# Performance work log

Hardware: AMD Instinct MI355X
Metric: run time of the kernel (lower is better)

The kernel has to match this reference:

```python
import jax, jax.numpy as jnp
import numpy as np

C = 256
CQK = C // 8  # query/key channels from Conv2d(in_dim, in_dim//8, 1)


def _cross_attn(x, y, qw, qb, kw, kb, vw, vb, gamma):
    # x, y: [B, C, H, W]; 1x1 convs are channel matmuls
    B, Cc, H, W = x.shape
    N = H * W
    xf = x.reshape(B, Cc, N)
    yf = y.reshape(B, Cc, N)
    q = jnp.einsum('oc,bcn->bno', qw, xf) + qb  # [B, N, CQK]
    k = jnp.einsum('oc,bcn->bon', kw, yf) + kb[:, None]  # [B, CQK, N]
    energy = jnp.einsum('bnc,bcm->bnm', q, k)  # [B, N, N]
    attn = jax.nn.softmax(energy, axis=2)
    v = jnp.einsum('oc,bcn->bon', vw, yf) + vb[:, None]  # [B, C, N]
    out = jnp.einsum('bcm,bnm->bcn', v, attn)  # value @ attention^T
    out = out.reshape(B, Cc, H, W)
    return gamma * out + x


def setup_inputs() -> dict:
    key = jax.random.key(0)
    ks = jax.random.split(key, 16)
    B, H, W = 4, 64, 64
    s = 1.0 / np.sqrt(C)
    d = {
        'x': jax.random.normal(ks[0], (B, C, H, W), jnp.float32),
        'y': jax.random.normal(ks[1], (B, C, H, W), jnp.float32),
        'z': jax.random.normal(ks[2], (B, C, H, W), jnp.float32),
        'q1_w': jax.random.normal(ks[3], (CQK, C), jnp.float32) * s,
        'q1_b': jax.random.normal(ks[4], (CQK,), jnp.float32) * s,
        'k1_w': jax.random.normal(ks[5], (CQK, C), jnp.float32) * s,
        'k1_b': jax.random.normal(ks[6], (CQK,), jnp.float32) * s,
        'v1_w': jax.random.normal(ks[7], (C, C), jnp.float32) * s,
        'v1_b': jax.random.normal(ks[8], (C,), jnp.float32) * s,
        'gamma1': jax.random.normal(ks[9], (1,), jnp.float32) * 0.1,
        'q2_w': jax.random.normal(ks[10], (CQK, C), jnp.float32) * s,
        'q2_b': jax.random.normal(ks[11], (CQK,), jnp.float32) * s,
        'k2_w': jax.random.normal(ks[12], (CQK, C), jnp.float32) * s,
        'k2_b': jax.random.normal(ks[13], (CQK,), jnp.float32) * s,
        'v2_w': jax.random.normal(ks[14], (C, C), jnp.float32) * s,
        'v2_b': jax.random.normal(ks[15], (C,), jnp.float32) * s,
        'gamma2': jax.random.normal(jax.random.fold_in(key, 99), (1,), jnp.float32) * 0.1,
    }
    return d


def reference(x, y, z, q1_w, q1_b, k1_w, k1_b, v1_w, v1_b, gamma1,
              q2_w, q2_b, k2_w, k2_b, v2_w, v2_b, gamma2):
    out1 = _cross_attn(x, y, q1_w, q1_b, k1_w, k1_b, v1_w, v1_b, gamma1)
    out2 = _cross_attn(out1, z, q2_w, q2_b, k2_w, k2_b, v2_w, v2_b, gamma2)
    return out2
```

## Files before the change

kernel.cpp:

```cpp
#include <hip/hip_runtime.h>
#include <hip/hip_bf16.h>

#define NSEQ 4096
#define CDIM 256
#define CQKD 32
#define LOG2E 1.4426950408889634f

typedef float v4f __attribute__((ext_vector_type(4)));
typedef float v16f __attribute__((ext_vector_type(16)));
typedef short v8s __attribute__((ext_vector_type(8)));
typedef unsigned long long u64;

__device__ __forceinline__ float exp2_(float x) {
#if __has_builtin(__builtin_amdgcn_exp2f)
  return __builtin_amdgcn_exp2f(x);
#else
  float r;
  __asm__("v_exp_f32 %0, %1" : "=v"(r) : "v"(x));
  return r;
#endif
}

__device__ __forceinline__ unsigned short f2bf(float x) {
  unsigned u = __builtin_bit_cast(unsigned, x);
  unsigned r = (u + 0x7FFFu + ((u >> 16) & 1u)) >> 16;
  return (unsigned short)r;
}
__device__ __forceinline__ float bf2f(unsigned short s) {
  unsigned u = ((unsigned)s) << 16;
  return __builtin_bit_cast(float, u);
}
__device__ __forceinline__ unsigned int pack_bf16(float a, float b) {
#if __has_builtin(__builtin_amdgcn_cvt_pk_bf16_f32)
  typedef __bf16 v2bf __attribute__((ext_vector_type(2)));
  v2bf r = __builtin_amdgcn_cvt_pk_bf16_f32(a, b);
  return __builtin_bit_cast(unsigned int, r);
#else
  return ((unsigned)f2bf(b) << 16) | (unsigned)f2bf(a);
#endif
}

__device__ __forceinline__ unsigned char f2e4m3(float x) {
  unsigned u = __builtin_bit_cast(unsigned, x);
  unsigned s = (u >> 24) & 0x80u;
  unsigned au = u & 0x7fffffffu;
  if (au > 0x43e00000u) return (unsigned char)(s | 0x7eu);
  if (au < 0x3c800000u) {
    float ax = __builtin_bit_cast(float, au);
    int q = (int)(ax * 512.0f + 0.5f);
    if (q > 7) q = 7;
    return (unsigned char)(s | (unsigned)q);
  }
  int e = (int)((au >> 23) & 0xffu) - 127 + 7;
  unsigned m = au & 0x7fffffu;
  unsigned mr = m + 0x7ffffu + ((m >> 20) & 1u);
  if (mr >= 0x800000u) { mr -= 0x800000u; e += 1; if (e >= 16) return (unsigned char)(s | 0x7e); }
  return (unsigned char)(s | ((unsigned)e << 3) | (mr >> 20));
}
__device__ __forceinline__ unsigned int pack4_fp8(float a, float b, float c, float d) {
#if __has_builtin(__builtin_amdgcn_cvt_pk_fp8_f32)
  int v = 0;
  v = __builtin_amdgcn_cvt_pk_fp8_f32(a, b, v, false);
  v = __builtin_amdgcn_cvt_pk_fp8_f32(c, d, v, true);
  return (unsigned int)v;
#else
  return (unsigned)f2e4m3(a) | ((unsigned)f2e4m3(b) << 8) |
         ((unsigned)f2e4m3(c) << 16) | ((unsigned)f2e4m3(d) << 24);
#endif
}

__device__ __forceinline__ void barrier_lds() {
  __asm__ __volatile__("s_waitcnt lgkmcnt(0)\n\ts_barrier" ::: "memory");
}

__global__ __launch_bounds__(256) void convw_kernel(
    const float* __restrict__ q1w, const float* __restrict__ k1w,
    const float* __restrict__ k2w, const float* __restrict__ q2w,
    const float* __restrict__ v1w, const float* __restrict__ v2w,
    unsigned short* __restrict__ W) {
  const int s = blockIdx.x * 256 + threadIdx.x;
  const float* src;
  int o, ch0;
  size_t obase;
  float scale = 1.0f;
  if (s < 3072) {
    const int wsel = s >> 10, r = s & 1023;
    src = wsel == 0 ? q1w : (wsel == 1 ? k1w : k2w);
    const int ot = r >> 9, cb = (r >> 6) & 7, lane = r & 63;
    o = ot * 16 + (lane & 15);
    ch0 = cb * 32 + ((lane >> 4) & 3) * 8;
    obase = (size_t)wsel * 8192 + (size_t)r * 8;
  } else if (s < 19456) {
    const int s2 = s - 3072, which = s2 >> 13, r = s2 & 8191;
    src = which == 0 ? v1w : v2w;
    const int ot = r >> 9, cb = (r >> 6) & 7, lane = r & 63;
    o = ot * 16 + (lane & 15);
    ch0 = cb * 32 + ((lane >> 4) & 3) * 8;
    obase = 32768 + (size_t)which * 65536 + (size_t)r * 8;
  } else {
    const int r = s - 19456;
    src = q2w;
    const int lane = r & 63;
    o = lane & 31;
    ch0 = (r >> 6) * 16 + (lane >> 5) * 8;
    obase = 24576 + (size_t)r * 8;
    scale = LOG2E;
  }
#pragma unroll
  for (int j = 0; j < 8; ++j)
    W[obase + j] = f2bf(src[o * CDIM + ch0 + j] * scale);
}

__global__ __launch_bounds__(256) void prep_kernel(
    const float* __restrict__ x, const float* __restrict__ y,
    const float* __restrict__ z, const unsigned short* __restrict__ Wbf,
    const float* __restrict__ q1b, const float* __restrict__ k1b,
    const float* __restrict__ k2b, const float* __restrict__ v1b,
    const float* __restrict__ v2b, unsigned short* __restrict__ Q1,
    unsigned short* __restrict__ K1, unsigned short* __restrict__ K2,
    unsigned char* __restrict__ V1, unsigned char* __restrict__ V2) {
  __shared__ unsigned short t[256][72];
  __shared__ unsigned short Kt[64][40];
  const int src = blockIdx.z;
  const float* in = src == 0 ? x : (src == 1 ? y : z);
  const int b = blockIdx.y;
  const int n0 = blockIdx.x * 64;
  const int tid = threadIdx.x, lane = tid & 63, w = tid >> 6;
  const int quad = lane >> 4, r15 = lane & 15, l31 = lane & 31, lh = lane >> 5;
  const float* ip = in + (size_t)(b * CDIM) * NSEQ + n0;
  {
    const int chb = tid >> 4, c4 = (tid & 15) * 4;
#pragma unroll
    for (int p = 0; p < 16; ++p) {
      const int ch = p * 16 + chb;
      float4 v = *(const float4*)(ip + (size_t)ch * NSEQ + c4);
      uint2 pk;
      pk.x = pack_bf16(v.x, v.y);
      pk.y = pack_bf16(v.z, v.w);
      *(uint2*)&t[ch][c4] = pk;
    }
  }
  __syncthreads();
  v8s af[8];
#pragma unroll
  for (int cb = 0; cb < 8; ++cb) {
    union { unsigned short e[8]; v8s v; } u;
#pragma unroll
    for (int j = 0; j < 8; ++j) u.e[j] = t[cb * 32 + quad * 8 + j][w * 16 + r15];
    af[cb] = u.v;
  }
  const int nt = blockIdx.x * 4 + w;
  const unsigned short* Wqk = Wbf + src * 8192;
  v4f a0 = {0.f, 0.f, 0.f, 0.f}, a1 = a0;
#pragma unroll
  for (int cb = 0; cb < 8; ++cb) {
    v8s b0 = *(const v8s*)(Wqk + (size_t)cb * 512 + lane * 8);
    v8s b1 = *(const v8s*)(Wqk + (size_t)(8 + cb) * 512 + lane * 8);
    a0 = __builtin_amdgcn_mfma_f32_16x16x32_bf16(af[cb], b0, a0, 0, 0, 0);
    a1 = __builtin_amdgcn_mfma_f32_16x16x32_bf16(af[cb], b1, a1, 0, 0, 0);
  }
  if (src == 0) {
#pragma unroll
    for (int r = 0; r < 4; ++r) {
      Q1[((size_t)b * NSEQ + nt * 16 + quad * 4 + r) * CQKD + r15] =
          f2bf((a0[r] + q1b[r15]) * LOG2E);
      Q1[((size_t)b * NSEQ + nt * 16 + quad * 4 + r) * CQKD + 16 + r15] =
          f2bf((a1[r] + q1b[16 + r15]) * LOG2E);
    }
    return;
  }
  const float* kbias = src == 1 ? k1b : k2b;
#pragma unroll
  for (int r = 0; r < 4; ++r) {
    Kt[w * 16 + quad * 4 + r][r15] = f2bf(a0[r] + kbias[r15]);
    Kt[w * 16 + quad * 4 + r][16 + r15] = f2bf(a1[r] + kbias[16 + r15]);
  }
  const unsigned short* Wv = Wbf + 32768 + (src - 1) * 65536;
  const float* vbias = src == 1 ? v1b : v2b;
  v4f vacc[16];
#pragma unroll
  for (int ot = 0; ot < 16; ++ot) vacc[ot] = (v4f){0.f, 0.f, 0.f, 0.f};
#pragma unroll
  for (int cb = 0; cb < 8; ++cb) {
    const v8s afc = af[cb];
#pragma unroll
    for (int ot = 0; ot < 16; ++ot) {
      v8s bf = *(const v8s*)(Wv + (size_t)(ot * 8 + cb) * 512 + lane * 8);
      vacc[ot] = __builtin_amdgcn_mfma_f32_16x16x32_bf16(afc, bf, vacc[ot], 0, 0, 0);
    }
  }
  __syncthreads();
  unsigned char* Vt8 = (unsigned char*)t;
#pragma unroll
  for (int ot = 0; ot < 16; ++ot) {
    const int ch = ot * 16 + r15;
    const float bv = vbias[ch];
    *(unsigned int*)&Vt8[(size_t)ch * 72 + w * 16 + quad * 4] =
        pack4_fp8(vacc[ot][0] + bv, vacc[ot][1] + bv, vacc[ot][2] + bv, vacc[ot][3] + bv);
  }
  {
    unsigned short* Kout = (src == 1 ? K1 : K2) + (size_t)b * (NSEQ / 16) * 512;
    *(v8s*)(Kout + ((size_t)nt * 64 + lane) * 8) = *(const v8s*)&Kt[w * 16 + r15][quad * 8];
  }
  __syncthreads();
  unsigned char* Vout = (src == 1 ? V1 : V2) + (size_t)b * (NSEQ / 16) * 8 * 512;
#pragma unroll
  for (int chb = 0; chb < 8; ++chb)
    *(u64*)(Vout + (((size_t)nt * 8 + chb) * 64 + lane) * 8) =
        *(const u64*)&Vt8[(size_t)(chb * 32 + l31) * 72 + w * 16 + lh * 8];
}


__device__ __forceinline__ void max_pass(
    const unsigned short* __restrict__ Kp, const v8s qf[2], int w, int lane,
    float (*lbuf)[32], float m[2]) {
  const v4f vzero4 = {0.f, 0.f, 0.f, 0.f};
  const int r15 = lane & 15;
  const unsigned short* Kl = Kp + (size_t)w * 512 + lane * 8;
  v8s kA = *(const v8s*)(Kl);
  m[0] = -3.0e38f;
  m[1] = -3.0e38f;
  for (int kt = 0; kt < 32; ++kt) {
    v8s kB = *(const v8s*)(Kl + (size_t)((kt + 1) & 31) * 4096);
#pragma unroll
    for (int qt = 0; qt < 2; ++qt) {
      v4f st = __builtin_amdgcn_mfma_f32_16x16x32_bf16(kA, qf[qt], vzero4, 0, 0, 0);
      m[qt] = fmaxf(m[qt], fmaxf(fmaxf(st[0], st[1]), fmaxf(st[2], st[3])));
    }
    kA = kB;
  }
#pragma unroll
  for (int qt = 0; qt < 2; ++qt) {
    m[qt] = fmaxf(m[qt], __shfl_xor(m[qt], 16));
    m[qt] = fmaxf(m[qt], __shfl_xor(m[qt], 32));
  }
  if (lane < 16) {
#pragma unroll
    for (int qt = 0; qt < 2; ++qt) lbuf[w][qt * 16 + lane] = m[qt];
  }
  __syncthreads();
#pragma unroll
  for (int qt = 0; qt < 2; ++qt) {
    float mm = lbuf[0][qt * 16 + r15];
#pragma unroll
    for (int ww = 1; ww < 8; ++ww) mm = fmaxf(mm, lbuf[ww][qt * 16 + r15]);
    m[qt] = mm;
  }
  __syncthreads();
}

__device__ __forceinline__ void attn_tile(
    const unsigned short* __restrict__ Kl, const unsigned char* __restrict__ Vl,
    unsigned char* __restrict__ P, const v8s qf[2], const float m[2], int w, int lane,
    int pbuf, int tn, const v8s kfu, const u64* vfu, v8s& kfn, u64* vfn,
    v16f& acc, float lsum[2]) {
  const v4f vzero4 = {0.f, 0.f, 0.f, 0.f};
  const int quad = (lane >> 4) & 3, r15 = lane & 15;
  const int l31 = lane & 31, lh = lane >> 5;
  kfn = *(const v8s*)(Kl + (size_t)tn * 4096);
#pragma unroll
  for (int s = 0; s < 8; ++s)
    vfn[s] = *(const u64*)(Vl + (size_t)tn * 32768 + s * 4096);
  unsigned char* pw = P + pbuf * 4352 + w * 16 + quad * 4;
#pragma unroll
  for (int qt = 0; qt < 2; ++qt) {
    v4f st = __builtin_amdgcn_mfma_f32_16x16x32_bf16(kfu, qf[qt], vzero4, 0, 0, 0);
    float e0 = exp2_(st[0] - m[qt]), e1 = exp2_(st[1] - m[qt]);
    float e2 = exp2_(st[2] - m[qt]), e3 = exp2_(st[3] - m[qt]);
    lsum[qt] += (e0 + e1) + (e2 + e3);
    *(unsigned int*)(pw + (size_t)(qt * 16 + r15) * 136) = pack4_fp8(e0, e1, e2, e3);
  }
  barrier_lds();
  const unsigned char* pb = P + pbuf * 4352;
#pragma unroll
  for (int s = 0; s < 8; ++s) {
    long pf0 = (long)*(const u64*)(pb + (size_t)l31 * 136 + s * 16 + lh * 8);
    acc = __builtin_amdgcn_mfma_f32_32x32x16_fp8_fp8((long)vfu[s], pf0, acc, 0, 0, 0);
  }
}

__device__ __forceinline__ void attn_loop(
    const unsigned short* __restrict__ Kp, const unsigned char* __restrict__ Vp,
    unsigned char* __restrict__ P, const v8s qf[2], const float m[2], int w, int lane,
    v16f& acc, float lsum[2]) {
  const unsigned short* Kl = Kp + (size_t)w * 512 + lane * 8;
  const unsigned char* Vl = Vp + (size_t)w * 512 + lane * 8;
  v8s kA, kB;
  u64 vA[8], vB[8];
  kA = *(const v8s*)(Kl);
#pragma unroll
  for (int s = 0; s < 8; ++s) vA[s] = *(const u64*)(Vl + (size_t)s * 4096);
  for (int kt = 0; kt < 32; kt += 2) {
    attn_tile(Kl, Vl, P, qf, m, w, lane, 0, (kt + 1) & 31, kA, vA, kB, vB, acc, lsum);
    attn_tile(Kl, Vl, P, qf, m, w, lane, 1, (kt + 2) & 31, kB, vB, kA, vA, acc, lsum);
  }
}

__global__ __launch_bounds__(512, 2) void fused_attn_kernel(
    const unsigned short* __restrict__ Q1g, const unsigned short* __restrict__ K1g,
    const unsigned char* __restrict__ V1g, const unsigned short* __restrict__ K2g,
    const unsigned char* __restrict__ V2g, const unsigned short* __restrict__ W2g,
    const float* __restrict__ x, const float* __restrict__ q2b,
    const float* __restrict__ g1p, const float* __restrict__ g2p,
    float* __restrict__ outp) {
  __shared__ __align__(16) unsigned char P[2 * 4352];
  __shared__ __align__(16) unsigned short out1T[32 * 264];
  __shared__ __align__(16) unsigned short q2s[32 * 32];
  __shared__ float lbuf[8][32];

  const int tid = threadIdx.x;
  const int lane = tid & 63;
  const int w = tid >> 6;
  const int quad = lane >> 4;
  const int r15 = lane & 15;
  const int l31 = lane & 31, lh = lane >> 5;
  const int b = blockIdx.x & 3;
  const int n0 = (blockIdx.x >> 2) * 32;

  const float g1 = g1p[0];
  const float g2 = g2p[0];

  const unsigned short* Qp  = Q1g + (size_t)b * NSEQ * CQKD;
  const unsigned short* K1p = K1g + (size_t)b * (NSEQ / 16) * 512;
  const unsigned short* K2p = K2g + (size_t)b * (NSEQ / 16) * 512;
  const unsigned char* V1p  = V1g + (size_t)b * (NSEQ / 16) * 8 * 512;
  const unsigned char* V2p  = V2g + (size_t)b * (NSEQ / 16) * 8 * 512;

  v8s qf[2];
#pragma unroll
  for (int qt = 0; qt < 2; ++qt)
    qf[qt] = *(const v8s*)(Qp + (n0 + qt * 16 + r15) * CQKD + quad * 8);

  v16f acc = (v16f)(0.f);
  float lsum[2] = {0.f, 0.f};
  float m[2];

  max_pass(K1p, qf, w, lane, lbuf, m);
  attn_loop(K1p, V1p, P, qf, m, w, lane, acc, lsum);
#pragma unroll
  for (int qt = 0; qt < 2; ++qt) {
    lsum[qt] += __shfl_xor(lsum[qt], 16);
    lsum[qt] += __shfl_xor(lsum[qt], 32);
  }
  __syncthreads();
  if (lane < 16) {
#pragma unroll
    for (int qt = 0; qt < 2; ++qt) lbuf[w][qt * 16 + lane] = lsum[qt];
  }
  __syncthreads();
  float rinv;
  {
    float d = 0.f;
#pragma unroll
    for (int ww = 0; ww < 8; ++ww) d += lbuf[ww][l31];
    rinv = 1.0f / d;
  }
  {
    const int q = l31;
#pragma unroll
    for (int rg = 0; rg < 4; ++rg) {
      const int c = w * 32 + 8 * rg + 4 * lh;
      float o0 = g1 * (acc[rg * 4 + 0] * rinv) + x[((size_t)b * CDIM + c + 0) * NSEQ + n0 + q];
      float o1 = g1 * (acc[rg * 4 + 1] * rinv) + x[((size_t)b * CDIM + c + 1) * NSEQ + n0 + q];
      float o2 = g1 * (acc[rg * 4 + 2] * rinv) + x[((size_t)b * CDIM + c + 2) * NSEQ + n0 + q];
      float o3 = g1 * (acc[rg * 4 + 3] * rinv) + x[((size_t)b * CDIM + c + 3) * NSEQ + n0 + q];
      uint2 pk;
      pk.x = pack_bf16(o0, o1);
      pk.y = pack_bf16(o2, o3);
      *(uint2*)(out1T + (size_t)q * 264 + c) = pk;
    }
  }
  __syncthreads();

  if (w == 0) {
    v16f qacc = (v16f)(0.f);
#pragma unroll
    for (int s = 0; s < 16; ++s) {
      v8s af = *(const v8s*)(W2g + (size_t)(s * 64 + lane) * 8);
      v8s bf = *(const v8s*)(out1T + (size_t)l31 * 264 + s * 16 + lh * 8);
      qacc = __builtin_amdgcn_mfma_f32_32x32x16_bf16(af, bf, qacc, 0, 0, 0);
    }
#pragma unroll
    for (int rg = 0; rg < 4; ++rg) {
      const int o = 8 * rg + 4 * lh;
      uint2 pk;
      pk.x = pack_bf16(qacc[rg * 4 + 0] + q2b[o + 0] * LOG2E, qacc[rg * 4 + 1] + q2b[o + 1] * LOG2E);
      pk.y = pack_bf16(qacc[rg * 4 + 2] + q2b[o + 2] * LOG2E, qacc[rg * 4 + 3] + q2b[o + 3] * LOG2E);
      *(uint2*)(q2s + (size_t)l31 * 32 + o) = pk;
    }
  }
  __syncthreads();

#pragma unroll
  for (int qt = 0; qt < 2; ++qt)
    qf[qt] = *(const v8s*)(q2s + (qt * 16 + r15) * 32 + quad * 8);
  acc = (v16f)(0.f);
  lsum[0] = 0.f;
  lsum[1] = 0.f;
  max_pass(K2p, qf, w, lane, lbuf, m);
  attn_loop(K2p, V2p, P, qf, m, w, lane, acc, lsum);
#pragma unroll
  for (int qt = 0; qt < 2; ++qt) {
    lsum[qt] += __shfl_xor(lsum[qt], 16);
    lsum[qt] += __shfl_xor(lsum[qt], 32);
  }
  __syncthreads();
  if (lane < 16) {
#pragma unroll
    for (int qt = 0; qt < 2; ++qt) lbuf[w][qt * 16 + lane] = lsum[qt];
  }
  __syncthreads();
  {
    float d = 0.f;
#pragma unroll
    for (int ww = 0; ww < 8; ++ww) d += lbuf[ww][l31];
    rinv = 1.0f / d;
  }
  {
    const int q = l31;
#pragma unroll
    for (int rg = 0; rg < 4; ++rg) {
      const int c = w * 32 + 8 * rg + 4 * lh;
#pragma unroll
      for (int i = 0; i < 4; ++i) {
        float res = bf2f(out1T[(size_t)q * 264 + c + i]);
        outp[((size_t)b * CDIM + c + i) * NSEQ + n0 + q] =
            g2 * (acc[rg * 4 + i] * rinv) + res;
      }
    }
  }
}

extern "C" void kernel_launch(void* const* d_in, const int* in_sizes, int n_in,
                              void* d_out, int out_size, void* d_ws, size_t ws_size,
                              hipStream_t stream) {
  const float* x   = (const float*)d_in[0];
  const float* y   = (const float*)d_in[1];
  const float* z   = (const float*)d_in[2];
  const float* q1w = (const float*)d_in[3];
  const float* q1b = (const float*)d_in[4];
  const float* k1w = (const float*)d_in[5];
  const float* k1b = (const float*)d_in[6];
  const float* v1w = (const float*)d_in[7];
  const float* v1b = (const float*)d_in[8];
  const float* g1  = (const float*)d_in[9];
  const float* q2w = (const float*)d_in[10];
  const float* q2b = (const float*)d_in[11];
  const float* k2w = (const float*)d_in[12];
  const float* k2b = (const float*)d_in[13];
  const float* v2w = (const float*)d_in[14];
  const float* v2b = (const float*)d_in[15];
  const float* g2  = (const float*)d_in[16];
  char* ws = (char*)d_ws;
  unsigned short* Wbf = (unsigned short*)(ws);
  unsigned short* Q1  = (unsigned short*)(ws + 327680);
  unsigned short* K1  = (unsigned short*)(ws + 1376256);
  unsigned short* K2  = (unsigned short*)(ws + 2424832);
  unsigned char*  V1  = (unsigned char*)(ws + 3473408);
  unsigned char*  V2  = (unsigned char*)(ws + 7667712);
  float* outp = (float*)d_out;

  convw_kernel<<<dim3(80), 256, 0, stream>>>(q1w, k1w, k2w, q2w, v1w, v2w, Wbf);
  prep_kernel<<<dim3(64, 4, 3), 256, 0, stream>>>(x, y, z, Wbf, q1b, k1b, k2b, v1b,
                                                  v2b, Q1, K1, K2, V1, V2);
  fused_attn_kernel<<<dim3(512), 512, 0, stream>>>(Q1, K1, V1, K2, V2, Wbf + 24576, x,
                                                   q2b, g1, g2, outp);
}
```

Before: 237.2 us.

## Warp-specialize attention loop into QK/softmax producers and PV consumers

Splits the eight waves into four producer waves that compute QK scores, exponentiate and write fp8 P tiles, and four consumer waves that run the PV MFMAs over two channel blocks each. P grows to four LDS buffers, giving a deeper ring between the two groups, and consumer waves raise their scheduling priority around the MFMAs. The max pass gains a two-tile-ahead K prefetch, and launch bounds are raised to ask for four blocks per CU. The aim is to overlap the exp/softmax work with the PV matrix math, at the cost of more registers per consumer wave (32 u64 V fragments plus two accumulators) and an occupancy target that may not be reachable.

```diff
diff --git a/kernel.cpp b/kernel.cpp
--- a/kernel.cpp
+++ b/kernel.cpp
@@ -211,23 +211,26 @@
 }
 
 
-__device__ __forceinline__ void max_pass(
+__device__ __forceinline__ void max_pass8(
     const unsigned short* __restrict__ Kp, const v8s qf[2], int w, int lane,
     float (*lbuf)[32], float m[2]) {
   const v4f vzero4 = {0.f, 0.f, 0.f, 0.f};
   const int r15 = lane & 15;
   const unsigned short* Kl = Kp + (size_t)w * 512 + lane * 8;
   v8s kA = *(const v8s*)(Kl);
+  v8s kB = *(const v8s*)(Kl + 4096);
   m[0] = -3.0e38f;
   m[1] = -3.0e38f;
+#pragma unroll 2
   for (int kt = 0; kt < 32; ++kt) {
-    v8s kB = *(const v8s*)(Kl + (size_t)((kt + 1) & 31) * 4096);
+    v8s kC = *(const v8s*)(Kl + (size_t)((kt + 2) & 31) * 4096);
 #pragma unroll
     for (int qt = 0; qt < 2; ++qt) {
       v4f st = __builtin_amdgcn_mfma_f32_16x16x32_bf16(kA, qf[qt], vzero4, 0, 0, 0);
       m[qt] = fmaxf(m[qt], fmaxf(fmaxf(st[0], st[1]), fmaxf(st[2], st[3])));
     }
     kA = kB;
+    kB = kC;
   }
 #pragma unroll
   for (int qt = 0; qt < 2; ++qt) {
@@ -249,61 +252,117 @@
   __syncthreads();
 }
 
-__device__ __forceinline__ void attn_tile(
-    const unsigned short* __restrict__ Kl, const unsigned char* __restrict__ Vl,
-    unsigned char* __restrict__ P, const v8s qf[2], const float m[2], int w, int lane,
-    int pbuf, int tn, const v8s kfu, const u64* vfu, v8s& kfn, u64* vfn,
-    v16f& acc, float lsum[2]) {
+__device__ __forceinline__ void s_slice(
+    unsigned char* __restrict__ P, int pbuf, int sl, const v8s kf, const v8s qf[2],
+    const float m[2], int lane, float lsum[2]) {
   const v4f vzero4 = {0.f, 0.f, 0.f, 0.f};
-  const int quad = (lane >> 4) & 3, r15 = lane & 15;
-  const int l31 = lane & 31, lh = lane >> 5;
-  kfn = *(const v8s*)(Kl + (size_t)tn * 4096);
-#pragma unroll
-  for (int s = 0; s < 8; ++s)
-    vfn[s] = *(const u64*)(Vl + (size_t)tn * 32768 + s * 4096);
-  unsigned char* pw = P + pbuf * 4352 + w * 16 + quad * 4;
+  const int quad = lane >> 4, r15 = lane & 15;
+  unsigned char* pw = P + pbuf * 4352 + sl * 16 + quad * 4;
 #pragma unroll
   for (int qt = 0; qt < 2; ++qt) {
-    v4f st = __builtin_amdgcn_mfma_f32_16x16x32_bf16(kfu, qf[qt], vzero4, 0, 0, 0);
+    v4f st = __builtin_amdgcn_mfma_f32_16x16x32_bf16(kf, qf[qt], vzero4, 0, 0, 0);
     float e0 = exp2_(st[0] - m[qt]), e1 = exp2_(st[1] - m[qt]);
     float e2 = exp2_(st[2] - m[qt]), e3 = exp2_(st[3] - m[qt]);
     lsum[qt] += (e0 + e1) + (e2 + e3);
     *(unsigned int*)(pw + (size_t)(qt * 16 + r15) * 136) = pack4_fp8(e0, e1, e2, e3);
   }
-  barrier_lds();
+}
+
+__device__ __forceinline__ void pv_tile2(
+    const unsigned char* __restrict__ P, int pbuf, const u64 vf[16], int lane,
+    v16f acc[2]) {
+  const int l31 = lane & 31, lh = lane >> 5;
   const unsigned char* pb = P + pbuf * 4352;
+  __builtin_amdgcn_s_setprio(1);
 #pragma unroll
   for (int s = 0; s < 8; ++s) {
-    long pf0 = (long)*(const u64*)(pb + (size_t)l31 * 136 + s * 16 + lh * 8);
-    acc = __builtin_amdgcn_mfma_f32_32x32x16_fp8_fp8((long)vfu[s], pf0, acc, 0, 0, 0);
-  }
+    long pf = (long)*(const u64*)(pb + (size_t)l31 * 136 + s * 16 + lh * 8);
+    acc[0] = __builtin_amdgcn_mfma_f32_32x32x16_fp8_fp8((long)vf[2 * s], pf, acc[0], 0, 0, 0);
+    acc[1] = __builtin_amdgcn_mfma_f32_32x32x16_fp8_fp8((long)vf[2 * s + 1], pf, acc[1], 0, 0, 0);
+  }
+  __builtin_amdgcn_s_setprio(0);
 }
 
 __device__ __forceinline__ void attn_loop(
     const unsigned short* __restrict__ Kp, const unsigned char* __restrict__ Vp,
     unsigned char* __restrict__ P, const v8s qf[2], const float m[2], int w, int lane,
-    v16f& acc, float lsum[2]) {
-  const unsigned short* Kl = Kp + (size_t)w * 512 + lane * 8;
-  const unsigned char* Vl = Vp + (size_t)w * 512 + lane * 8;
-  v8s kA, kB;
-  u64 vA[8], vB[8];
-  kA = *(const v8s*)(Kl);
-#pragma unroll
-  for (int s = 0; s < 8; ++s) vA[s] = *(const u64*)(Vl + (size_t)s * 4096);
-  for (int kt = 0; kt < 32; kt += 2) {
-    attn_tile(Kl, Vl, P, qf, m, w, lane, 0, (kt + 1) & 31, kA, vA, kB, vB, acc, lsum);
-    attn_tile(Kl, Vl, P, qf, m, w, lane, 1, (kt + 2) & 31, kB, vB, kA, vA, acc, lsum);
-  }
-}
-
-__global__ __launch_bounds__(512, 2) void fused_attn_kernel(
+    v16f acc[2], float lsum[2]) {
+  if (w < 4) {
+    const unsigned short* Kl0 = Kp + (size_t)(2 * w) * 512 + lane * 8;
+    const unsigned short* Kl1 = Kp + (size_t)(2 * w + 1) * 512 + lane * 8;
+    v8s ka0 = *(const v8s*)(Kl0);
+    v8s ka1 = *(const v8s*)(Kl1);
+    v8s kb0 = *(const v8s*)(Kl0 + 4096);
+    v8s kb1 = *(const v8s*)(Kl1 + 4096);
+    s_slice(P, 0, 2 * w, ka0, qf, m, lane, lsum);
+    s_slice(P, 0, 2 * w + 1, ka1, qf, m, lane, lsum);
+    ka0 = *(const v8s*)(Kl0 + 2 * 4096);
+    ka1 = *(const v8s*)(Kl1 + 2 * 4096);
+    s_slice(P, 1, 2 * w, kb0, qf, m, lane, lsum);
+    s_slice(P, 1, 2 * w + 1, kb1, qf, m, lane, lsum);
+    kb0 = *(const v8s*)(Kl0 + 3 * 4096);
+    kb1 = *(const v8s*)(Kl1 + 3 * 4096);
+    barrier_lds();
+#pragma unroll 1
+    for (int p = 1; p < 16; ++p) {
+      const int bs = (p & 1) * 2;
+      s_slice(P, bs, 2 * w, ka0, qf, m, lane, lsum);
+      s_slice(P, bs, 2 * w + 1, ka1, qf, m, lane, lsum);
+      ka0 = *(const v8s*)(Kl0 + (size_t)((2 * p + 2) & 31) * 4096);
+      ka1 = *(const v8s*)(Kl1 + (size_t)((2 * p + 2) & 31) * 4096);
+      s_slice(P, bs + 1, 2 * w, kb0, qf, m, lane, lsum);
+      s_slice(P, bs + 1, 2 * w + 1, kb1, qf, m, lane, lsum);
+      kb0 = *(const v8s*)(Kl0 + (size_t)((2 * p + 3) & 31) * 4096);
+      kb1 = *(const v8s*)(Kl1 + (size_t)((2 * p + 3) & 31) * 4096);
+      barrier_lds();
+    }
+    barrier_lds();
+  } else {
+    const int pvw = w - 4;
+    const unsigned char* Vl = Vp + (size_t)(2 * pvw) * 512 + lane * 8;
+    u64 v0[16], v1[16];
+#pragma unroll
+    for (int s = 0; s < 8; ++s) {
+      v0[2 * s] = *(const u64*)(Vl + (size_t)s * 4096);
+      v0[2 * s + 1] = *(const u64*)(Vl + (size_t)s * 4096 + 512);
+    }
+#pragma unroll
+    for (int s = 0; s < 8; ++s) {
+      v1[2 * s] = *(const u64*)(Vl + 32768 + (size_t)s * 4096);
+      v1[2 * s + 1] = *(const u64*)(Vl + 32768 + (size_t)s * 4096 + 512);
+    }
+    barrier_lds();
+#pragma unroll 1
+    for (int p = 0; p < 15; ++p) {
+      const int bs = (p & 1) * 2;
+      pv_tile2(P, bs, v0, lane, acc);
+#pragma unroll
+      for (int s = 0; s < 8; ++s) {
+        v0[2 * s] = *(const u64*)(Vl + (size_t)(2 * p + 2) * 32768 + s * 4096);
+        v0[2 * s + 1] = *(const u64*)(Vl + (size_t)(2 * p + 2) * 32768 + s * 4096 + 512);
+      }
+      pv_tile2(P, bs + 1, v1, lane, acc);
+#pragma unroll
+      for (int s = 0; s < 8; ++s) {
+        v1[2 * s] = *(const u64*)(Vl + (size_t)(2 * p + 3) * 32768 + s * 4096);
+        v1[2 * s + 1] = *(const u64*)(Vl + (size_t)(2 * p + 3) * 32768 + s * 4096 + 512);
+      }
+      barrier_lds();
+    }
+    pv_tile2(P, 2, v0, lane, acc);
+    pv_tile2(P, 3, v1, lane, acc);
+    barrier_lds();
+  }
+}
+
+__global__ __launch_bounds__(512, 4) void fused_attn_kernel(
     const unsigned short* __restrict__ Q1g, const unsigned short* __restrict__ K1g,
     const unsigned char* __restrict__ V1g, const unsigned short* __restrict__ K2g,
     const unsigned char* __restrict__ V2g, const unsigned short* __restrict__ W2g,
     const float* __restrict__ x, const float* __restrict__ q2b,
     const float* __restrict__ g1p, const float* __restrict__ g2p,
     float* __restrict__ outp) {
-  __shared__ __align__(16) unsigned char P[2 * 4352];
+  __shared__ __align__(16) unsigned char P[4 * 4352];
   __shared__ __align__(16) unsigned short out1T[32 * 264];
   __shared__ __align__(16) unsigned short q2s[32 * 32];
   __shared__ float lbuf[8][32];
@@ -331,43 +390,49 @@
   for (int qt = 0; qt < 2; ++qt)
     qf[qt] = *(const v8s*)(Qp + (n0 + qt * 16 + r15) * CQKD + quad * 8);
 
-  v16f acc = (v16f)(0.f);
+  v16f acc[2];
   float lsum[2] = {0.f, 0.f};
   float m[2];
-
-  max_pass(K1p, qf, w, lane, lbuf, m);
+  acc[0] = (v16f)(0.f); acc[1] = (v16f)(0.f);
+
+  max_pass8(K1p, qf, w, lane, lbuf, m);
   attn_loop(K1p, V1p, P, qf, m, w, lane, acc, lsum);
-#pragma unroll
-  for (int qt = 0; qt < 2; ++qt) {
-    lsum[qt] += __shfl_xor(lsum[qt], 16);
-    lsum[qt] += __shfl_xor(lsum[qt], 32);
-  }
-  __syncthreads();
-  if (lane < 16) {
-#pragma unroll
-    for (int qt = 0; qt < 2; ++qt) lbuf[w][qt * 16 + lane] = lsum[qt];
+  if (w < 4) {
+#pragma unroll
+    for (int qt = 0; qt < 2; ++qt) {
+      lsum[qt] += __shfl_xor(lsum[qt], 16);
+      lsum[qt] += __shfl_xor(lsum[qt], 32);
+    }
+    if (lane < 16) {
+#pragma unroll
+      for (int qt = 0; qt < 2; ++qt) lbuf[w][qt * 16 + lane] = lsum[qt];
+    }
   }
   __syncthreads();
   float rinv;
   {
     float d = 0.f;
 #pragma unroll
-    for (int ww = 0; ww < 8; ++ww) d += lbuf[ww][l31];
+    for (int ww = 0; ww < 4; ++ww) d += lbuf[ww][l31];
     rinv = 1.0f / d;
   }
-  {
+  if (w >= 4) {
     const int q = l31;
 #pragma unroll
-    for (int rg = 0; rg < 4; ++rg) {
-      const int c = w * 32 + 8 * rg + 4 * lh;
-      float o0 = g1 * (acc[rg * 4 + 0] * rinv) + x[((size_t)b * CDIM + c + 0) * NSEQ + n0 + q];
-      float o1 = g1 * (acc[rg * 4 + 1] * rinv) + x[((size_t)b * CDIM + c + 1) * NSEQ + n0 + q];
-      float o2 = g1 * (acc[rg * 4 + 2] * rinv) + x[((size_t)b * CDIM + c + 2) * NSEQ + n0 + q];
-      float o3 = g1 * (acc[rg * 4 + 3] * rinv) + x[((size_t)b * CDIM + c + 3) * NSEQ + n0 + q];
-      uint2 pk;
-      pk.x = pack_bf16(o0, o1);
-      pk.y = pack_bf16(o2, o3);
-      *(uint2*)(out1T + (size_t)q * 264 + c) = pk;
+    for (int h = 0; h < 2; ++h) {
+      const int cw = ((w - 4) * 2 + h) * 32;
+#pragma unroll
+      for (int rg = 0; rg < 4; ++rg) {
+        const int c = cw + 8 * rg + 4 * lh;
+        float o0 = g1 * (acc[h][rg * 4 + 0] * rinv) + x[((size_t)b * CDIM + c + 0) * NSEQ + n0 + q];
+        float o1 = g1 * (acc[h][rg * 4 + 1] * rinv) + x[((size_t)b * CDIM + c + 1) * NSEQ + n0 + q];
+        float o2 = g1 * (acc[h][rg * 4 + 2] * rinv) + x[((size_t)b * CDIM + c + 2) * NSEQ + n0 + q];
+        float o3 = g1 * (acc[h][rg * 4 + 3] * rinv) + x[((size_t)b * CDIM + c + 3) * NSEQ + n0 + q];
+        uint2 pk;
+        pk.x = pack_bf16(o0, o1);
+        pk.y = pack_bf16(o2, o3);
+        *(uint2*)(out1T + (size_t)q * 264 + c) = pk;
+      }
     }
   }
   __syncthreads();
@@ -394,38 +459,43 @@
 #pragma unroll
   for (int qt = 0; qt < 2; ++qt)
     qf[qt] = *(const v8s*)(q2s + (qt * 16 + r15) * 32 + quad * 8);
-  acc = (v16f)(0.f);
+  acc[0] = (v16f)(0.f); acc[1] = (v16f)(0.f);
   lsum[0] = 0.f;
   lsum[1] = 0.f;
-  max_pass(K2p, qf, w, lane, lbuf, m);
+  max_pass8(K2p, qf, w, lane, lbuf, m);
   attn_loop(K2p, V2p, P, qf, m, w, lane, acc, lsum);
-#pragma unroll
-  for (int qt = 0; qt < 2; ++qt) {
-    lsum[qt] += __shfl_xor(lsum[qt], 16);
-    lsum[qt] += __shfl_xor(lsum[qt], 32);
-  }
-  __syncthreads();
-  if (lane < 16) {
-#pragma unroll
-    for (int qt = 0; qt < 2; ++qt) lbuf[w][qt * 16 + lane] = lsum[qt];
+  if (w < 4) {
+#pragma unroll
+    for (int qt = 0; qt < 2; ++qt) {
+      lsum[qt] += __shfl_xor(lsum[qt], 16);
+      lsum[qt] += __shfl_xor(lsum[qt], 32);
+    }
+    if (lane < 16) {
+#pragma unroll
+      for (int qt = 0; qt < 2; ++qt) lbuf[w][qt * 16 + lane] = lsum[qt];
+    }
   }
   __syncthreads();
   {
     float d = 0.f;
 #pragma unroll
-    for (int ww = 0; ww < 8; ++ww) d += lbuf[ww][l31];
+    for (int ww = 0; ww < 4; ++ww) d += lbuf[ww][l31];
     rinv = 1.0f / d;
   }
-  {
+  if (w >= 4) {
     const int q = l31;
 #pragma unroll
-    for (int rg = 0; rg < 4; ++rg) {
-      const int c = w * 32 + 8 * rg + 4 * lh;
-#pragma unroll
-      for (int i = 0; i < 4; ++i) {
-        float res = bf2f(out1T[(size_t)q * 264 + c + i]);
-        outp[((size_t)b * CDIM + c + i) * NSEQ + n0 + q] =
-            g2 * (acc[rg * 4 + i] * rinv) + res;
+    for (int h = 0; h < 2; ++h) {
+      const int cw = ((w - 4) * 2 + h) * 32;
+#pragma unroll
+      for (int rg = 0; rg < 4; ++rg) {
+        const int c = cw + 8 * rg + 4 * lh;
+#pragma unroll
+        for (int i = 0; i < 4; ++i) {
+          float res = bf2f(out1T[(size_t)q * 264 + c + i]);
+          outp[((size_t)b * CDIM + c + i) * NSEQ + n0 + q] =
+              g2 * (acc[h][rg * 4 + i] * rinv) + res;
+        }
       }
     }
   }
```

Result: no change. 235.0 us (-0.9%).
